# Optimization experiments

Hardware: AMD Instinct MI355X
Metric: run time of the kernel (lower is better)

Reference implementation:

```python
import jax, jax.numpy as jnp
import numpy as np

B, H, W = 8, 64, 64
DIM, HEADS, WS = 512, 8, 8
C2 = DIM // 2            # attention branch channels
HD = C2 // HEADS         # head dim = 32
NH, NW = H // WS, W // WS
WIN = WS * WS            # tokens per window = 64
SCALE = HD ** -0.5
EPS = 1e-5


def layer_norm(x, g, b):
    m = jnp.mean(x, axis=-1, keepdims=True)
    v = jnp.mean((x - m) ** 2, axis=-1, keepdims=True)
    return (x - m) * jax.lax.rsqrt(v + EPS) * g + b


def dwconv3x3(x, w, b=None):
    # x: (N, C, h, w); w: (C, 1, 3, 3) depthwise
    out = jax.lax.conv_general_dilated(
        x, w, window_strides=(1, 1), padding='SAME',
        feature_group_count=x.shape[1],
        dimension_numbers=('NCHW', 'OIHW', 'NCHW'))
    if b is not None:
        out = out + b[None, :, None, None]
    return out


def setup_inputs() -> dict:
    key = jax.random.key(0)
    ks = jax.random.split(key, 8)
    r = lambda k, s: (jax.random.normal(k, s, jnp.float32) * 0.02)
    return {
        'x': jax.random.normal(ks[0], (B, H * W, DIM), jnp.float32),
        'norm1_g': jnp.ones((DIM,), jnp.float32),
        'norm1_b': jnp.zeros((DIM,), jnp.float32),
        'qkv_w': r(ks[1], (C2, 3 * C2)),
        'qkv_b': jnp.zeros((3 * C2,), jnp.float32),
        'lepe_w': r(ks[2], (C2, 1, 3, 3)),
        'lepe_b': jnp.zeros((C2,), jnp.float32),
        'convloc_w': r(ks[3], (C2, 1, 3, 3)),
        'proj_w': r(ks[4], (DIM, DIM)),
        'proj_b': jnp.zeros((DIM,), jnp.float32),
        'norm2_g': jnp.ones((DIM,), jnp.float32),
        'norm2_b': jnp.zeros((DIM,), jnp.float32),
        'fc1_w': r(ks[5], (DIM, 4 * DIM)),
        'fc1_b': jnp.zeros((4 * DIM,), jnp.float32),
        'fc2_w': r(ks[6], (4 * DIM, DIM)),
        'fc2_b': jnp.zeros((DIM,), jnp.float32),
    }


def reference(x, norm1_g, norm1_b, qkv_w, qkv_b, lepe_w, lepe_b, convloc_w,
              proj_w, proj_b, norm2_g, norm2_b, fc1_w, fc1_b, fc2_w, fc2_b):
    img = layer_norm(x, norm1_g, norm1_b)                      # (B, L, DIM)

    # qkv from first half of channels
    qkv = img[..., :C2] @ qkv_w + qkv_b                        # (B, L, 3*C2)
    qkv = qkv.reshape(B, H * W, 3, C2)
    q, k, v = qkv[:, :, 0], qkv[:, :, 1], qkv[:, :, 2]

    def win6(t):  # (B, L, C2) -> (B, NH, NW, WS, WS, C2)
        return t.reshape(B, NH, WS, NW, WS, C2).transpose(0, 1, 3, 2, 4, 5)

    def to_heads(t6):
        return t6.reshape(-1, WIN, HEADS, HD).transpose(0, 2, 1, 3)

    qh = to_heads(win6(q)) * SCALE
    kh = to_heads(win6(k))

    # v + LePE: depthwise 3x3 conv applied per-window
    vw = win6(v).transpose(0, 1, 2, 5, 3, 4).reshape(-1, C2, WS, WS)
    lepe = dwconv3x3(vw, lepe_w, lepe_b)                       # (nWin, C2, WS, WS)
    vh = vw.reshape(-1, HEADS, HD, WIN).transpose(0, 1, 3, 2)
    leh = lepe.reshape(-1, HEADS, HD, WIN).transpose(0, 1, 3, 2)

    attn = jax.nn.softmax(jnp.einsum('nhqd,nhkd->nhqk', qh, kh), axis=-1)
    o = jnp.einsum('nhqk,nhkd->nhqd', attn, vh) + leh

    # merge windows back to (B, L, C2)
    o = o.transpose(0, 2, 1, 3).reshape(B, NH, NW, WS, WS, C2)
    o = o.transpose(0, 1, 3, 2, 4, 5).reshape(B, H * W, C2)

    # parallel depthwise-conv branch on second half of channels (no bias)
    x2 = img[..., C2:].transpose(0, 2, 1).reshape(B, C2, H, W)
    x2 = dwconv3x3(x2, convloc_w)
    x2 = x2.reshape(B, C2, H * W).transpose(0, 2, 1)

    local = jnp.concatenate([o, x2], axis=-1) @ proj_w + proj_b
    x = x + local

    # MLP_FFN: Linear -> GELU -> Linear
    h = jax.nn.gelu(layer_norm(x, norm2_g, norm2_b) @ fc1_w + fc1_b,
                    approximate=False)
    x = x + (h @ fc2_w + fc2_b)
    return x
```

## Files before the change

### kernel.cpp

```cpp
#include <hip/hip_runtime.h>
#include <cstdint>
#include <cstddef>

typedef unsigned short u16;
typedef __attribute__((ext_vector_type(8))) short short8;
typedef __attribute__((ext_vector_type(4))) float f32x4;

#define DIM 512
#define C2  256
#define HD  32
#define SCALE_Q 0.17677669529663689f

__device__ __forceinline__ float bf2f(u16 u){ return __uint_as_float(((unsigned)u) << 16); }
__device__ __forceinline__ u16 f2bf(float f){
  unsigned u = __float_as_uint(f);
  unsigned r = (u + 0x7FFFu + ((u >> 16) & 1u)) >> 16;
  return (u16)r;
}

__device__ __forceinline__ f32x4 mfma16(short8 a, short8 b, f32x4 c){
  return __builtin_amdgcn_mfma_f32_16x16x32_bf16(a, b, c, 0, 0, 0);
}

__device__ __forceinline__ void gload16(const u16* g, u16* l){
  __builtin_amdgcn_global_load_lds((const __attribute__((address_space(1))) void*)g,
                                   (__attribute__((address_space(3))) void*)l, 16, 0, 0);
}

__device__ __forceinline__ float gelu_f(float v){
  float e = __expf(-1.702f * v);
  return v * __builtin_amdgcn_rcpf(1.0f + e);
}

__global__ __launch_bounds__(256) void transpose_all_kernel(
    const float* __restrict__ qkv_w, const float* __restrict__ proj_w,
    const float* __restrict__ fc1_w, const float* __restrict__ fc2_w,
    u16* __restrict__ qkv_wT, u16* __restrict__ proj_wT,
    u16* __restrict__ fc1_wT, u16* __restrict__ fc2_wT){
  __shared__ u16 Tl[32][33];
  int b = blockIdx.x;
  const float* W; u16* WT; int K, N, nx, ti;
  if (b < 192)      { W = qkv_w;  WT = qkv_wT;  K = 256;  N = 768;  nx = 24; ti = b; }
  else if (b < 448) { W = proj_w; WT = proj_wT; K = 512;  N = 512;  nx = 16; ti = b - 192; }
  else if (b < 1472){ W = fc1_w;  WT = fc1_wT;  K = 512;  N = 2048; nx = 64; ti = b - 448; }
  else              { W = fc2_w;  WT = fc2_wT;  K = 2048; N = 512;  nx = 16; ti = b - 1472; }
  int n0 = (ti % nx) * 32, k0 = (ti / nx) * 32;
  int tx = threadIdx.x & 31, ty = threadIdx.x >> 5;
#pragma unroll
  for (int i = 0; i < 4; i++){
    int k = ty * 4 + i;
    Tl[k][tx] = f2bf(W[(size_t)(k0 + k) * N + n0 + tx]);
  }
  __syncthreads();
#pragma unroll
  for (int i = 0; i < 4; i++){
    int n = ty * 4 + i;
    WT[(size_t)(n0 + n) * K + k0 + tx] = Tl[tx][n];
  }
}

__global__ __launch_bounds__(256) void ln_kernel(const float* __restrict__ x, const float* __restrict__ g,
                                                 const float* __restrict__ bta, u16* __restrict__ out){
  int row  = blockIdx.x * 4 + (threadIdx.x >> 6);
  int lane = threadIdx.x & 63;
  size_t base = (size_t)row * DIM + lane * 8;
  float4 v0 = *(const float4*)(x + base);
  float4 v1 = *(const float4*)(x + base + 4);
  float f[8] = {v0.x, v0.y, v0.z, v0.w, v1.x, v1.y, v1.z, v1.w};
  float s = 0.f;
#pragma unroll
  for (int j = 0; j < 8; j++) s += f[j];
#pragma unroll
  for (int m = 1; m < 64; m <<= 1) s += __shfl_xor(s, m, 64);
  float mean = s * (1.0f / DIM);
  float vs = 0.f;
#pragma unroll
  for (int j = 0; j < 8; j++){ float d = f[j] - mean; vs += d * d; }
#pragma unroll
  for (int m = 1; m < 64; m <<= 1) vs += __shfl_xor(vs, m, 64);
  float rstd = rsqrtf(vs * (1.0f / DIM) + 1e-5f);
  float4 g0 = *(const float4*)(g + lane * 8);
  float4 g1 = *(const float4*)(g + lane * 8 + 4);
  float4 b0 = *(const float4*)(bta + lane * 8);
  float4 b1 = *(const float4*)(bta + lane * 8 + 4);
  float gg[8] = {g0.x, g0.y, g0.z, g0.w, g1.x, g1.y, g1.z, g1.w};
  float bb[8] = {b0.x, b0.y, b0.z, b0.w, b1.x, b1.y, b1.z, b1.w};
  short8 o;
#pragma unroll
  for (int j = 0; j < 8; j++){
    float r = (f[j] - mean) * rstd * gg[j] + bb[j];
    o[j] = (short)f2bf(r);
  }
  *(short8*)(out + base) = o;
}

template<int EPI, bool OUT_BF16>
__device__ __forceinline__ void gemm8_body(
    const u16* __restrict__ A, int lda,
    const u16* __restrict__ WT,
    const float* __restrict__ bias,
    const float* R, int ldr,
    void* Cv, int ldc, int K)
{
  __shared__ u16 Al[2][2][256 * 32];
  __shared__ u16 Bl[2][2][256 * 32];
  const int tid = threadIdx.x;
  const int l   = tid & 63;
  const int w   = tid >> 6;
  const int wr  = w >> 2;
  const int wc  = w & 3;
  const int l16 = l & 15, lhi = l >> 4;

  const int gx = gridDim.x;
  int bid = blockIdx.y * gx + blockIdx.x;
  int nwg = gx * gridDim.y;
  int sw  = (nwg & 7) ? bid : ((bid & 7) * (nwg >> 3) + (bid >> 3));
  const int col0 = (sw % gx) * 256, row0 = (sw / gx) * 256;
  const int NT = K >> 6;

  const int srow = w * 16 + (l >> 2);
  const int cs   = (((l & 3) ^ ((l >> 3) & 3)) * 8);
  const u16* pA = A  + (size_t)(row0 + srow) * lda + cs;
  const u16* pB = WT + (size_t)(col0 + srow) * K  + cs;
  const size_t a128 = (size_t)128 * lda, b128 = (size_t)128 * K;

  auto stageA = [&](int tt, int hh){
    if (tt < NT){
      size_t go = (size_t)tt * 64 + (size_t)hh * 32;
      gload16(pA + go,        &Al[tt & 1][hh][(w * 16) * 32]);
      gload16(pA + a128 + go, &Al[tt & 1][hh][(128 + w * 16) * 32]);
    }
  };
  auto stageB = [&](int tt, int hh){
    if (tt < NT){
      size_t go = (size_t)tt * 64 + (size_t)hh * 32;
      gload16(pB + go,        &Bl[tt & 1][hh][(w * 16) * 32]);
      gload16(pB + b128 + go, &Bl[tt & 1][hh][(128 + w * 16) * 32]);
    }
  };

  const int rdo = l16 * 32 + (lhi ^ ((l16 >> 1) & 3)) * 8;

  f32x4 acc[8][4] = {};
  short8 af[4], bf[4];

  stageA(0, 0); stageB(0, 0); stageA(0, 1); stageB(0, 1);
  stageA(1, 0); stageB(1, 0); stageA(1, 1); stageB(1, 1);
  asm volatile("s_waitcnt vmcnt(8)" ::: "memory");
  __builtin_amdgcn_sched_barrier(0);
  __builtin_amdgcn_s_barrier();

#define PHASE(BC, KH, QM, STAGES) do{                                                   \
    if ((QM) == 0){                                                                     \
      _Pragma("unroll")                                                                 \
      for (int n = 0; n < 4; n++)                                                       \
        bf[n] = *(const short8*)&Bl[BC][KH][(wc * 64 + n * 16) * 32 + rdo];             \
    }                                                                                   \
    _Pragma("unroll")                                                                   \
    for (int m = 0; m < 4; m++)                                                         \
      af[m] = *(const short8*)&Al[BC][KH][(wr * 128 + (QM) * 64 + m * 16) * 32 + rdo];  \
    STAGES;                                                                             \
    __builtin_amdgcn_s_barrier();                                                       \
    asm volatile("s_waitcnt lgkmcnt(0)" ::: "memory");                                  \
    __builtin_amdgcn_sched_barrier(0);                                                  \
    __builtin_amdgcn_s_setprio(1);                                                      \
    _Pragma("unroll")                                                                   \
    for (int m = 0; m < 4; m++)                                                         \
      _Pragma("unroll")                                                                 \
      for (int n = 0; n < 4; n++)                                                       \
        acc[(QM) * 4 + m][n] = mfma16(bf[n], af[m], acc[(QM) * 4 + m][n]);              \
    __builtin_amdgcn_s_setprio(0);                                                      \
    __builtin_amdgcn_s_barrier();                                                       \
  }while(0)

  for (int t = 0; t < NT; t++){
    const int bc = t & 1;
    PHASE(bc, 0, 0, (void)0);
    PHASE(bc, 0, 1, stageB(t + 2, 0));
    PHASE(bc, 1, 0, stageA(t + 2, 0));
    PHASE(bc, 1, 1, stageB(t + 2, 1));
    stageA(t + 2, 1);
    if (t + 2 < NT) asm volatile("s_waitcnt vmcnt(8)" ::: "memory");
    else            asm volatile("s_waitcnt vmcnt(0)" ::: "memory");
    __builtin_amdgcn_sched_barrier(0);
    __builtin_amdgcn_s_barrier();
  }
#undef PHASE

  float4 bvs[4];
#pragma unroll
  for (int n = 0; n < 4; n++)
    bvs[n] = *(const float4*)&bias[col0 + wc * 64 + n * 16 + lhi * 4];
#pragma unroll
  for (int mq = 0; mq < 8; mq++){
    int grow = row0 + wr * 128 + mq * 16 + l16;
#pragma unroll
    for (int n = 0; n < 4; n++){
      int gcol = col0 + wc * 64 + n * 16 + lhi * 4;
      float4 vv = { acc[mq][n][0] + bvs[n].x, acc[mq][n][1] + bvs[n].y,
                    acc[mq][n][2] + bvs[n].z, acc[mq][n][3] + bvs[n].w };
      if constexpr (EPI == 1){
        float4 rv = *(const float4*)&R[(size_t)grow * ldr + gcol];
        vv.x += rv.x; vv.y += rv.y; vv.z += rv.z; vv.w += rv.w;
      }
      if constexpr (EPI == 2){
        vv.x = gelu_f(vv.x); vv.y = gelu_f(vv.y); vv.z = gelu_f(vv.z); vv.w = gelu_f(vv.w);
      }
      if constexpr (OUT_BF16){
        ushort4 o4 = { f2bf(vv.x), f2bf(vv.y), f2bf(vv.z), f2bf(vv.w) };
        *(ushort4*)&((u16*)Cv)[(size_t)grow * ldc + gcol] = o4;
      } else {
        *(float4*)&((float*)Cv)[(size_t)grow * ldc + gcol] = vv;
      }
    }
  }
}

__global__ __launch_bounds__(512, 2) void gemm_qkv_kernel(const u16* A, int lda, const u16* WT,
    const float* bias, const float* R, int ldr, void* Cv, int ldc, int K){
  gemm8_body<0, true>(A, lda, WT, bias, R, ldr, Cv, ldc, K);
}
__global__ __launch_bounds__(512, 2) void gemm_proj_kernel(const u16* A, int lda, const u16* WT,
    const float* bias, const float* R, int ldr, void* Cv, int ldc, int K){
  gemm8_body<1, false>(A, lda, WT, bias, R, ldr, Cv, ldc, K);
}
__global__ __launch_bounds__(512, 2) void gemm_fc1_kernel(const u16* A, int lda, const u16* WT,
    const float* bias, const float* R, int ldr, void* Cv, int ldc, int K){
  gemm8_body<2, true>(A, lda, WT, bias, R, ldr, Cv, ldc, K);
}
__global__ __launch_bounds__(512, 2) void gemm_fc2_kernel(const u16* A, int lda, const u16* WT,
    const float* bias, const float* R, int ldr, void* Cv, int ldc, int K){
  gemm8_body<1, false>(A, lda, WT, bias, R, ldr, Cv, ldc, K);
}

__global__ __launch_bounds__(64) void attn_kernel(
    const u16* __restrict__ qkv, const float* __restrict__ lw,
    const float* __restrict__ lb, u16* __restrict__ out)
{
  __shared__ float Ks[64][36];
  __shared__ float Vs[64][36];
  __shared__ float Wle[32][9];
  __shared__ float Lb[32];
  int head = blockIdx.x & 7, win = blockIdx.x >> 3;
  int wx = win & 7, wy = (win >> 3) & 7, b = win >> 6;
  int l  = threadIdx.x;
  int py = l >> 3, px = l & 7;
  size_t t = (size_t)b * 4096 + (size_t)(wy * 8 + py) * 64 + (wx * 8 + px);
  const u16* base = qkv + t * 768 + head * HD;

  float q[32];
#pragma unroll
  for (int j = 0; j < 32; j += 8){
    short8 vq = *(const short8*)(base + j);
    short8 vk = *(const short8*)(base + 256 + j);
    short8 vv = *(const short8*)(base + 512 + j);
#pragma unroll
    for (int e = 0; e < 8; e++){
      q[j + e]     = bf2f((u16)vq[e]) * SCALE_Q;
      Ks[l][j + e] = bf2f((u16)vk[e]);
      Vs[l][j + e] = bf2f((u16)vv[e]);
    }
  }
  for (int i = l; i < 288; i += 64) Wle[i / 9][i % 9] = lw[(head * 32 + i / 9) * 9 + (i % 9)];
  if (l < 32) Lb[l] = lb[head * 32 + l];
  __syncthreads();

  float sc[64];
  float mx = -1e30f;
#pragma unroll
  for (int k = 0; k < 64; k++){
    float s = 0.f;
#pragma unroll
    for (int d = 0; d < 32; d++) s += q[d] * Ks[k][d];
    sc[k] = s; mx = fmaxf(mx, s);
  }
  float sum = 0.f;
#pragma unroll
  for (int k = 0; k < 64; k++){ float e = __expf(sc[k] - mx); sc[k] = e; sum += e; }
  float inv = 1.0f / sum;
  float o[32];
#pragma unroll
  for (int d = 0; d < 32; d++) o[d] = 0.f;
#pragma unroll
  for (int k = 0; k < 64; k++){
    float p = sc[k] * inv;
#pragma unroll
    for (int d = 0; d < 32; d++) o[d] += p * Vs[k][d];
  }
#pragma unroll
  for (int ky = 0; ky < 3; ky++){
    int yy = py + ky - 1;
    if (yy < 0 || yy >= 8) continue;
#pragma unroll
    for (int kx = 0; kx < 3; kx++){
      int xx = px + kx - 1;
      if (xx < 0 || xx >= 8) continue;
      int kp = yy * 8 + xx;
#pragma unroll
      for (int d = 0; d < 32; d++) o[d] += Wle[d][ky * 3 + kx] * Vs[kp][d];
    }
  }
  u16* op = out + t * DIM + head * HD;
#pragma unroll
  for (int d = 0; d < 32; d += 4){
    ushort4 o4 = { f2bf(o[d] + Lb[d]), f2bf(o[d + 1] + Lb[d + 1]),
                   f2bf(o[d + 2] + Lb[d + 2]), f2bf(o[d + 3] + Lb[d + 3]) };
    *(ushort4*)&op[d] = o4;
  }
}

__global__ __launch_bounds__(256) void convloc_kernel(const u16* __restrict__ img,
    const float* __restrict__ w, u16* __restrict__ out){
  __shared__ float Wl[9 * 256];
  int tid = threadIdx.x;
  for (int i = tid; i < 2304; i += 256){
    int ch = i / 9, tp = i - ch * 9;
    Wl[tp * 256 + ch] = w[i];
  }
  __syncthreads();
  int c  = (tid & 63) * 4;
  int pq = tid >> 6;
  int p  = blockIdx.x * 4 + pq;
  int b  = p >> 12;
  int pi = p & 4095;
  int y = pi >> 6, x = pi & 63;
  float a0 = 0.f, a1 = 0.f, a2 = 0.f, a3 = 0.f;
#pragma unroll
  for (int ky = 0; ky < 3; ky++){
    int yy = y + ky - 1;
    if (yy < 0 || yy >= 64) continue;
#pragma unroll
    for (int kx = 0; kx < 3; kx++){
      int xx = x + kx - 1;
      if (xx < 0 || xx >= 64) continue;
      ushort4 v = *(const ushort4*)&img[((size_t)b * 4096 + yy * 64 + xx) * DIM + C2 + c];
      float4 wv = *(const float4*)&Wl[(ky * 3 + kx) * 256 + c];
      a0 += wv.x * bf2f(v.x); a1 += wv.y * bf2f(v.y);
      a2 += wv.z * bf2f(v.z); a3 += wv.w * bf2f(v.w);
    }
  }
  ushort4 o4 = { f2bf(a0), f2bf(a1), f2bf(a2), f2bf(a3) };
  *(ushort4*)&out[((size_t)b * 4096 + pi) * DIM + C2 + c] = o4;
}

extern "C" void kernel_launch(void* const* d_in, const int* in_sizes, int n_in,
                              void* d_out, int out_size, void* d_ws, size_t ws_size,
                              hipStream_t stream){
  const float* x      = (const float*)d_in[0];
  const float* n1g    = (const float*)d_in[1];
  const float* n1b    = (const float*)d_in[2];
  const float* qkv_w  = (const float*)d_in[3];
  const float* qkv_b  = (const float*)d_in[4];
  const float* lepe_w = (const float*)d_in[5];
  const float* lepe_b = (const float*)d_in[6];
  const float* conv_w = (const float*)d_in[7];
  const float* proj_w = (const float*)d_in[8];
  const float* proj_b = (const float*)d_in[9];
  const float* n2g    = (const float*)d_in[10];
  const float* n2b    = (const float*)d_in[11];
  const float* fc1_w  = (const float*)d_in[12];
  const float* fc1_b  = (const float*)d_in[13];
  const float* fc2_w  = (const float*)d_in[14];
  const float* fc2_b  = (const float*)d_in[15];
  float* out = (float*)d_out;

  char* ws = (char*)d_ws;
  u16* img     = (u16*)(ws + 0);
  u16* qkvb    = (u16*)(ws + 33554432ull);
  u16* localb  = (u16*)(ws + 83886080ull);
  u16* y       = (u16*)(ws + 0);
  u16* h       = (u16*)(ws + 33554432ull);
  u16* qkv_wT  = (u16*)(ws + 167772160ull);
  u16* proj_wT = (u16*)(ws + 167772160ull + 393216ull);
  u16* fc1_wT  = (u16*)(ws + 167772160ull + 393216ull + 524288ull);
  u16* fc2_wT  = (u16*)(ws + 167772160ull + 393216ull + 524288ull + 2097152ull);
  float* xa    = (float*)d_out;

  transpose_all_kernel<<<2496, 256, 0, stream>>>(qkv_w, proj_w, fc1_w, fc2_w,
                                                 qkv_wT, proj_wT, fc1_wT, fc2_wT);

  ln_kernel<<<8192, 256, 0, stream>>>(x, n1g, n1b, img);

  dim3 gq(3, 128);
  gemm_qkv_kernel<<<gq, 512, 0, stream>>>(img, DIM, qkv_wT, qkv_b, nullptr, 0, qkvb, 768, 256);

  attn_kernel<<<4096, 64, 0, stream>>>(qkvb, lepe_w, lepe_b, localb);
  convloc_kernel<<<8192, 256, 0, stream>>>(img, conv_w, localb);

  dim3 gp(2, 128);
  gemm_proj_kernel<<<gp, 512, 0, stream>>>(localb, DIM, proj_wT, proj_b, x, DIM, xa, DIM, 512);

  ln_kernel<<<8192, 256, 0, stream>>>(xa, n2g, n2b, y);

  dim3 g1(8, 128);
  gemm_fc1_kernel<<<g1, 512, 0, stream>>>(y, DIM, fc1_wT, fc1_b, nullptr, 0, h, 2048, 512);

  dim3 g2(2, 128);
  gemm_fc2_kernel<<<g2, 512, 0, stream>>>(h, 2048, fc2_wT, fc2_b, xa, DIM, out, DIM, 2048);
}
```

Before: 408.9 us.

## Rewrite window attention with bf16 MFMA, one block per window

The scalar per-thread window attention becomes an MFMA-based kernel. QK^T and PV run as 16x16x32 bf16 matrix instructions, with V transposed and probabilities staged through LDS in bf16. Each 256-thread block now handles one window, with each wave doing two heads, and LePE weights are loaded once per block. The cost is rounding the probabilities to bf16, and the LePE neighbour values are reread from global memory instead of shared memory.

```diff
diff --git a/kernel.cpp b/kernel.cpp
--- a/kernel.cpp
+++ b/kernel.cpp
@@ -233,79 +233,158 @@
   gemm8_body<1, false>(A, lda, WT, bias, R, ldr, Cv, ldc, K);
 }
 
-__global__ __launch_bounds__(64) void attn_kernel(
+__global__ __launch_bounds__(256) void attn_kernel(
     const u16* __restrict__ qkv, const float* __restrict__ lw,
     const float* __restrict__ lb, u16* __restrict__ out)
 {
-  __shared__ float Ks[64][36];
-  __shared__ float Vs[64][36];
-  __shared__ float Wle[32][9];
-  __shared__ float Lb[32];
-  int head = blockIdx.x & 7, win = blockIdx.x >> 3;
+  __shared__ u16  Vt[4][32 * 76];
+  __shared__ u16  Pl[4][64 * 76];
+  __shared__ float Wl[9 * 256];
+  __shared__ float Lb[256];
+  const int tid = threadIdx.x;
+  const int l   = tid & 63;
+  const int w   = tid >> 6;
+  const int l16 = l & 15, lhi = l >> 4;
+
+  int win = blockIdx.x;
   int wx = win & 7, wy = (win >> 3) & 7, b = win >> 6;
-  int l  = threadIdx.x;
-  int py = l >> 3, px = l & 7;
-  size_t t = (size_t)b * 4096 + (size_t)(wy * 8 + py) * 64 + (wx * 8 + px);
-  const u16* base = qkv + t * 768 + head * HD;
-
-  float q[32];
-#pragma unroll
-  for (int j = 0; j < 32; j += 8){
-    short8 vq = *(const short8*)(base + j);
-    short8 vk = *(const short8*)(base + 256 + j);
-    short8 vv = *(const short8*)(base + 512 + j);
-#pragma unroll
-    for (int e = 0; e < 8; e++){
-      q[j + e]     = bf2f((u16)vq[e]) * SCALE_Q;
-      Ks[l][j + e] = bf2f((u16)vk[e]);
-      Vs[l][j + e] = bf2f((u16)vv[e]);
-    }
-  }
-  for (int i = l; i < 288; i += 64) Wle[i / 9][i % 9] = lw[(head * 32 + i / 9) * 9 + (i % 9)];
-  if (l < 32) Lb[l] = lb[head * 32 + l];
+  auto trow = [&](int tok){
+    return (size_t)b * 4096 + (size_t)(wy * 8 + (tok >> 3)) * 64 + (wx * 8 + (tok & 7));
+  };
+
+  for (int i = tid; i < 2304; i += 256){
+    int ch = i / 9, tp = i - ch * 9;
+    Wl[tp * 256 + ch] = lw[i];
+  }
+  if (tid < 256) Lb[tid] = lb[tid];
   __syncthreads();
 
-  float sc[64];
-  float mx = -1e30f;
-#pragma unroll
-  for (int k = 0; k < 64; k++){
-    float s = 0.f;
-#pragma unroll
-    for (int d = 0; d < 32; d++) s += q[d] * Ks[k][d];
-    sc[k] = s; mx = fmaxf(mx, s);
-  }
-  float sum = 0.f;
-#pragma unroll
-  for (int k = 0; k < 64; k++){ float e = __expf(sc[k] - mx); sc[k] = e; sum += e; }
-  float inv = 1.0f / sum;
-  float o[32];
-#pragma unroll
-  for (int d = 0; d < 32; d++) o[d] = 0.f;
-#pragma unroll
-  for (int k = 0; k < 64; k++){
-    float p = sc[k] * inv;
-#pragma unroll
-    for (int d = 0; d < 32; d++) o[d] += p * Vs[k][d];
-  }
-#pragma unroll
-  for (int ky = 0; ky < 3; ky++){
-    int yy = py + ky - 1;
-    if (yy < 0 || yy >= 8) continue;
-#pragma unroll
-    for (int kx = 0; kx < 3; kx++){
-      int xx = px + kx - 1;
-      if (xx < 0 || xx >= 8) continue;
-      int kp = yy * 8 + xx;
-#pragma unroll
-      for (int d = 0; d < 32; d++) o[d] += Wle[d][ky * 3 + kx] * Vs[kp][d];
-    }
-  }
-  u16* op = out + t * DIM + head * HD;
-#pragma unroll
-  for (int d = 0; d < 32; d += 4){
-    ushort4 o4 = { f2bf(o[d] + Lb[d]), f2bf(o[d + 1] + Lb[d + 1]),
-                   f2bf(o[d + 2] + Lb[d + 2]), f2bf(o[d + 3] + Lb[d + 3]) };
-    *(ushort4*)&op[d] = o4;
+  u16* vt = Vt[w];
+  u16* pl = Pl[w];
+
+  for (int hi = 0; hi < 2; hi++){
+    const int h = w + hi * 4;
+    const int co = h * HD;
+
+    {
+      const u16* vp = qkv + trow(l) * 768 + 512 + co;
+#pragma unroll
+      for (int j = 0; j < 4; j++){
+        short8 v8 = *(const short8*)(vp + j * 8);
+#pragma unroll
+        for (int e = 0; e < 8; e++)
+          vt[(j * 8 + e) * 76 + l] = (u16)v8[e];
+      }
+    }
+
+    short8 Qf[4], Kf[4];
+#pragma unroll
+    for (int m = 0; m < 4; m++){
+      size_t r = trow(m * 16 + l16) * 768;
+      Qf[m] = *(const short8*)(qkv + r + co + lhi * 8);
+      Kf[m] = *(const short8*)(qkv + r + 256 + co + lhi * 8);
+    }
+
+    f32x4 s[4][4];
+#pragma unroll
+    for (int m = 0; m < 4; m++)
+#pragma unroll
+      for (int n = 0; n < 4; n++){
+        f32x4 z = {0.f, 0.f, 0.f, 0.f};
+        s[m][n] = mfma16(Kf[n], Qf[m], z);
+      }
+
+    float mx[4], sum[4], inv[4];
+#pragma unroll
+    for (int m = 0; m < 4; m++){
+      float mm = -1e30f;
+#pragma unroll
+      for (int n = 0; n < 4; n++)
+#pragma unroll
+        for (int i = 0; i < 4; i++){
+          s[m][n][i] *= SCALE_Q;
+          mm = fmaxf(mm, s[m][n][i]);
+        }
+      mm = fmaxf(mm, __shfl_xor(mm, 16, 64));
+      mm = fmaxf(mm, __shfl_xor(mm, 32, 64));
+      mx[m] = mm;
+      float ss = 0.f;
+#pragma unroll
+      for (int n = 0; n < 4; n++)
+#pragma unroll
+        for (int i = 0; i < 4; i++){
+          float e = __expf(s[m][n][i] - mm);
+          s[m][n][i] = e;
+          ss += e;
+        }
+      ss += __shfl_xor(ss, 16, 64);
+      ss += __shfl_xor(ss, 32, 64);
+      sum[m] = ss;
+      inv[m] = __builtin_amdgcn_rcpf(ss);
+    }
+
+#pragma unroll
+    for (int m = 0; m < 4; m++){
+      int q = m * 16 + l16;
+#pragma unroll
+      for (int n = 0; n < 4; n++){
+        ushort4 p4 = { f2bf(s[m][n][0] * inv[m]), f2bf(s[m][n][1] * inv[m]),
+                       f2bf(s[m][n][2] * inv[m]), f2bf(s[m][n][3] * inv[m]) };
+        *(ushort4*)&pl[q * 76 + n * 16 + lhi * 4] = p4;
+      }
+    }
+    short8 Pf[4][2], Vf[2][2];
+#pragma unroll
+    for (int m = 0; m < 4; m++)
+#pragma unroll
+      for (int st = 0; st < 2; st++)
+        Pf[m][st] = *(const short8*)&pl[(m * 16 + l16) * 76 + st * 32 + lhi * 8];
+#pragma unroll
+    for (int df = 0; df < 2; df++)
+#pragma unroll
+      for (int st = 0; st < 2; st++)
+        Vf[df][st] = *(const short8*)&vt[(df * 16 + l16) * 76 + st * 32 + lhi * 8];
+
+    f32x4 o[4][2];
+#pragma unroll
+    for (int m = 0; m < 4; m++)
+#pragma unroll
+      for (int df = 0; df < 2; df++){
+        f32x4 z = {0.f, 0.f, 0.f, 0.f};
+        z = mfma16(Vf[df][0], Pf[m][0], z);
+        o[m][df] = mfma16(Vf[df][1], Pf[m][1], z);
+      }
+
+#pragma unroll
+    for (int m = 0; m < 4; m++){
+      int q = m * 16 + l16;
+      int py = q >> 3, px = q & 7;
+#pragma unroll
+      for (int df = 0; df < 2; df++){
+        int dd = df * 16 + lhi * 4;
+#pragma unroll
+        for (int ky = 0; ky < 3; ky++){
+          int yy = py + ky - 1;
+          if (yy < 0 || yy >= 8) continue;
+#pragma unroll
+          for (int kx = 0; kx < 3; kx++){
+            int xx = px + kx - 1;
+            if (xx < 0 || xx >= 8) continue;
+            int kp = yy * 8 + xx;
+            ushort4 v4 = *(const ushort4*)(qkv + trow(kp) * 768 + 512 + co + dd);
+            float4 wv = *(const float4*)&Wl[(ky * 3 + kx) * 256 + co + dd];
+            o[m][df][0] += wv.x * bf2f(v4.x);
+            o[m][df][1] += wv.y * bf2f(v4.y);
+            o[m][df][2] += wv.z * bf2f(v4.z);
+            o[m][df][3] += wv.w * bf2f(v4.w);
+          }
+        }
+        float4 lbv = *(const float4*)&Lb[co + dd];
+        ushort4 o4 = { f2bf(o[m][df][0] + lbv.x), f2bf(o[m][df][1] + lbv.y),
+                       f2bf(o[m][df][2] + lbv.z), f2bf(o[m][df][3] + lbv.w) };
+        *(ushort4*)&out[trow(q) * DIM + co + dd] = o4;
+      }
+    }
   }
 }
 
@@ -384,7 +463,7 @@
   dim3 gq(3, 128);
   gemm_qkv_kernel<<<gq, 512, 0, stream>>>(img, DIM, qkv_wT, qkv_b, nullptr, 0, qkvb, 768, 256);
 
-  attn_kernel<<<4096, 64, 0, stream>>>(qkvb, lepe_w, lepe_b, localb);
+  attn_kernel<<<512, 256, 0, stream>>>(qkvb, lepe_w, lepe_b, localb);
   convloc_kernel<<<8192, 256, 0, stream>>>(img, conv_w, localb);
 
   dim3 gp(2, 128);
```

Result: faster. 390.8 us (-4.4%).
